# Performance work log

Measured on AMD Instinct MI355X. Metric: run time of the kernel, lower is better.

Reference implementation:

```python
import jax, jax.numpy as jnp
import numpy as np

BATCH = 262144
INPUT_DIM = 256
TREE_DEPTH = 10
NUM_LEAVES = 2 ** TREE_DEPTH


def _leaf_codes(depth):
    # codes[i, d] = d-th most-significant bit of i, matching format(i, f'0{depth}b')
    idx = np.arange(2 ** depth)[:, None]
    shifts = depth - 1 - np.arange(depth)[None, :]
    return jnp.asarray(((idx >> shifts) & 1).astype(np.float32))  # [L, D]


def setup_inputs() -> dict:
    key = jax.random.key(0)
    k1, k2, k3, k4 = jax.random.split(key, 4)
    x = jax.random.normal(k1, (BATCH, INPUT_DIM), dtype=jnp.float32)
    W = jax.random.normal(k2, (INPUT_DIM, TREE_DEPTH), dtype=jnp.float32) * (1.0 / np.sqrt(INPUT_DIM))
    b = jax.random.normal(k3, (TREE_DEPTH,), dtype=jnp.float32) * 0.01
    leaf_values = jax.random.normal(k4, (NUM_LEAVES,), dtype=jnp.float32)
    return {"x": x, "W": W, "b": b, "leaf_values": leaf_values}


def reference(x, W, b, leaf_values):
    depth = W.shape[1]
    codes = _leaf_codes(depth)                      # [L, D]
    decisions = jax.nn.sigmoid(x @ W + b)           # [B, D]
    # prod over depth of (d*c + (1-d)*(1-c)) without a [B, L, D] intermediate:
    # loop over the tiny depth axis (D=10), keeping only [B, L].
    leaf_probs = jnp.ones((x.shape[0], codes.shape[0]), dtype=x.dtype)
    for d in range(depth):
        dd = decisions[:, d][:, None]               # [B, 1]
        cc = codes[:, d][None, :]                   # [1, L]
        leaf_probs = leaf_probs * (dd * cc + (1.0 - dd) * (1.0 - cc))
    out = (leaf_probs * leaf_values).sum(axis=1, keepdims=True)  # [B, 1]
    return out
```

## Files before the change

### kernel.cpp

```cpp
#include <hip/hip_runtime.h>
#include <hip/hip_bf16.h>

#define TD 10
#define NCOL 256
#define GCOLS 32
#define NGRP (NCOL / GCOLS)

template <int LEVEL, int IDX>
__device__ __forceinline__ void fold(const float* __restrict__ lv,
                                     const float (&p)[TD], const float (&q)[TD],
                                     const float (&g)[16],
                                     float prefix, float& acc) {
  if constexpr (LEVEL == TD - 4) {
    const float* l16 = lv + 16 * IDX;
    float t = l16[0] * g[0];
#pragma unroll
    for (int k = 1; k < 16; ++k) t = fmaf(l16[k], g[k], t);
    acc = fmaf(prefix, t, acc);
  } else {
    fold<LEVEL + 1, 2 * IDX>(lv, p, q, g, prefix * q[LEVEL], acc);
    fold<LEVEL + 1, 2 * IDX + 1>(lv, p, q, g, prefix * p[LEVEL], acc);
  }
}

__global__ void __launch_bounds__(256, 4)
odt_kernel(const float* __restrict__ x, const float* __restrict__ W,
           const float* __restrict__ bias, const float* __restrict__ lv,
           float* __restrict__ out) {
  const int row = blockIdx.x * 256 + threadIdx.x;
  const float* __restrict__ xr = x + (size_t)row * NCOL;

  float4 buf[2][8];
#pragma unroll
  for (int j = 0; j < 8; ++j)
    buf[0][j] = *(const float4*)(xr + 4 * j);

  float sums[TD];
#pragma unroll
  for (int d = 0; d < TD; ++d) sums[d] = bias[d];

#pragma unroll
  for (int g = 0; g < NGRP; ++g) {
    if (g + 1 < NGRP) {
#pragma unroll
      for (int j = 0; j < 8; ++j)
        buf[(g + 1) & 1][j] =
            *(const float4*)(xr + (g + 1) * GCOLS + 4 * j);
    }
#pragma unroll
    for (int j = 0; j < 8; ++j) {
#pragma unroll
      for (int e = 0; e < 4; ++e) {
        const float xe = (&buf[g & 1][j].x)[e];
        const int col = g * GCOLS + 4 * j + e;
#pragma unroll
        for (int d = 0; d < TD; ++d)
          sums[d] = fmaf(xe, W[col * TD + d], sums[d]);
      }
    }
  }

  float p[TD], q[TD];
#pragma unroll
  for (int d = 0; d < TD; ++d) {
    const float s = 1.0f / (1.0f + __expf(-sums[d]));
    p[d] = s;
    q[d] = 1.0f - s;
  }

  float g[16];
  {
    float hA[4], hB[4];
    hA[0] = q[6] * q[7]; hA[1] = q[6] * p[7]; hA[2] = p[6] * q[7]; hA[3] = p[6] * p[7];
    hB[0] = q[8] * q[9]; hB[1] = q[8] * p[9]; hB[2] = p[8] * q[9]; hB[3] = p[8] * p[9];
#pragma unroll
    for (int o = 0; o < 16; ++o) g[o] = hA[o >> 2] * hB[o & 3];
  }

  float acc = 0.0f;
  fold<0, 0>(lv, p, q, g, 1.0f, acc);

  out[row] = acc;
}

extern "C" void kernel_launch(void* const* d_in, const int* in_sizes, int n_in,
                              void* d_out, int out_size, void* d_ws, size_t ws_size,
                              hipStream_t stream) {
  const float* x = (const float*)d_in[0];
  const float* W = (const float*)d_in[1];
  const float* b = (const float*)d_in[2];
  const float* lv = (const float*)d_in[3];
  float* out = (float*)d_out;

  const int batch = in_sizes[0] / NCOL;
  const int grid = batch / 256;
  odt_kernel<<<grid, 256, 0, stream>>>(x, W, b, lv, out);
}
```

Measured before the change: 64.64 us.

## Stage x tiles into LDS via direct global-to-LDS loads and split work across waves

Each block now processes 8 tiles of 64 rows. It stages every tile into LDS with global_load_lds, using a rotated column swizzle so that the row-per-lane reads avoid bank conflicts, and prefetches the next tile while the current one is being computed. Each of the 4 waves computes partial dot products over a quarter of the columns, and the partials are reduced through LDS. Each wave also evaluates a quarter of the leaf tree, and those results are summed at the end. The aim is coalesced global reads in place of per-thread strided row loads, plus less redundant per-thread leaf work, at the cost of extra barriers, 64KB+ of LDS and lower occupancy.

```diff
diff --git a/kernel.cpp b/kernel.cpp
--- a/kernel.cpp
+++ b/kernel.cpp
@@ -1,10 +1,16 @@
 #include <hip/hip_runtime.h>
-#include <hip/hip_bf16.h>
 
 #define TD 10
 #define NCOL 256
-#define GCOLS 32
-#define NGRP (NCOL / GCOLS)
+#define TROWS 64
+#define TILES 8
+#define ROWS_PER_BLOCK (TROWS * TILES)
+
+typedef const __attribute__((address_space(1))) void* as1_cvp;
+typedef __attribute__((address_space(3))) void* as3_vp;
+__device__ __forceinline__ void gload_lds16(const float* g, float* l) {
+  __builtin_amdgcn_global_load_lds((as1_cvp)(const void*)g, (as3_vp)(void*)l, 16, 0, 0);
+}
 
 template <int LEVEL, int IDX>
 __device__ __forceinline__ void fold(const float* __restrict__ lv,
@@ -23,64 +29,103 @@
   }
 }
 
-__global__ void __launch_bounds__(256, 4)
+__global__ void __launch_bounds__(256, 2)
 odt_kernel(const float* __restrict__ x, const float* __restrict__ W,
            const float* __restrict__ bias, const float* __restrict__ lv,
            float* __restrict__ out) {
-  const int row = blockIdx.x * 256 + threadIdx.x;
-  const float* __restrict__ xr = x + (size_t)row * NCOL;
+  __shared__ float xt[TROWS * NCOL];
+  __shared__ float ps[4][TROWS][12];
+  __shared__ float accs[4][TROWS];
 
-  float4 buf[2][8];
+  const int lane = threadIdx.x & 63;
+  const int wq = __builtin_amdgcn_readfirstlane(threadIdx.x >> 6);
+  const int blockrow0 = blockIdx.x * ROWS_PER_BLOCK;
+
+  auto stage = [&](int t) {
+    const int trow0 = blockrow0 + t * TROWS;
 #pragma unroll
-  for (int j = 0; j < 8; ++j)
-    buf[0][j] = *(const float4*)(xr + 4 * j);
+    for (int k = 0; k < 16; ++k) {
+      const int r = wq * 16 + k;
+      const float* src = x + (size_t)(trow0 + r) * NCOL + 4 * ((lane - r) & 63);
+      gload_lds16(src, &xt[r * NCOL]);
+    }
+  };
 
-  float sums[TD];
+  stage(0);
+
+  for (int t = 0; t < TILES; ++t) {
+    __syncthreads();
+
+    float sums[TD];
 #pragma unroll
-  for (int d = 0; d < TD; ++d) sums[d] = bias[d];
-
+    for (int d = 0; d < TD; ++d) sums[d] = 0.0f;
 #pragma unroll
-  for (int g = 0; g < NGRP; ++g) {
-    if (g + 1 < NGRP) {
-#pragma unroll
-      for (int j = 0; j < 8; ++j)
-        buf[(g + 1) & 1][j] =
-            *(const float4*)(xr + (g + 1) * GCOLS + 4 * j);
-    }
-#pragma unroll
-    for (int j = 0; j < 8; ++j) {
+    for (int i = 0; i < 16; ++i) {
+      const int pos = (16 * wq + i + lane) & 63;
+      const float4 xv = *(const float4*)&xt[lane * NCOL + 4 * pos];
 #pragma unroll
       for (int e = 0; e < 4; ++e) {
-        const float xe = (&buf[g & 1][j].x)[e];
-        const int col = g * GCOLS + 4 * j + e;
+        const float xe = (&xv.x)[e];
+        const int col = 64 * wq + 4 * i + e;
 #pragma unroll
         for (int d = 0; d < TD; ++d)
           sums[d] = fmaf(xe, W[col * TD + d], sums[d]);
       }
     }
+    {
+      float* pp = &ps[wq][lane][0];
+      *(float4*)(pp)     = make_float4(sums[0], sums[1], sums[2], sums[3]);
+      *(float4*)(pp + 4) = make_float4(sums[4], sums[5], sums[6], sums[7]);
+      *(float2*)(pp + 8) = make_float2(sums[8], sums[9]);
+    }
+
+    __syncthreads();
+
+    if (t + 1 < TILES) stage(t + 1);
+
+    float tot[TD];
+#pragma unroll
+    for (int d = 0; d < TD; ++d) tot[d] = bias[d];
+#pragma unroll
+    for (int wp = 0; wp < 4; ++wp) {
+      const float* qq = &ps[wp][lane][0];
+      const float4 a = *(const float4*)(qq);
+      const float4 b = *(const float4*)(qq + 4);
+      const float2 c = *(const float2*)(qq + 8);
+      tot[0] += a.x; tot[1] += a.y; tot[2] += a.z; tot[3] += a.w;
+      tot[4] += b.x; tot[5] += b.y; tot[6] += b.z; tot[7] += b.w;
+      tot[8] += c.x; tot[9] += c.y;
+    }
+
+    float p[TD], q[TD];
+#pragma unroll
+    for (int d = 0; d < TD; ++d) {
+      const float sg = 1.0f / (1.0f + __expf(-tot[d]));
+      p[d] = sg;
+      q[d] = 1.0f - sg;
+    }
+
+    float g[16];
+    {
+      float hA[4], hB[4];
+      hA[0] = q[6] * q[7]; hA[1] = q[6] * p[7]; hA[2] = p[6] * q[7]; hA[3] = p[6] * p[7];
+      hB[0] = q[8] * q[9]; hB[1] = q[8] * p[9]; hB[2] = p[8] * q[9]; hB[3] = p[8] * p[9];
+#pragma unroll
+      for (int o = 0; o < 16; ++o) g[o] = hA[o >> 2] * hB[o & 3];
+    }
+
+    float acc = 0.0f;
+    const float pref = ((wq & 2) ? p[0] : q[0]) * ((wq & 1) ? p[1] : q[1]);
+    fold<2, 0>(lv + 256 * wq, p, q, g, pref, acc);
+    accs[wq][lane] = acc;
+
+    __syncthreads();
+
+    if (wq == 0) {
+      const float o = accs[0][lane] + accs[1][lane] + accs[2][lane] + accs[3][lane];
+      out[blockrow0 + t * TROWS + lane] = o;
+    }
   }
-
-  float p[TD], q[TD];
-#pragma unroll
-  for (int d = 0; d < TD; ++d) {
-    const float s = 1.0f / (1.0f + __expf(-sums[d]));
-    p[d] = s;
-    q[d] = 1.0f - s;
-  }
-
-  float g[16];
-  {
-    float hA[4], hB[4];
-    hA[0] = q[6] * q[7]; hA[1] = q[6] * p[7]; hA[2] = p[6] * q[7]; hA[3] = p[6] * p[7];
-    hB[0] = q[8] * q[9]; hB[1] = q[8] * p[9]; hB[2] = p[8] * q[9]; hB[3] = p[8] * p[9];
-#pragma unroll
-    for (int o = 0; o < 16; ++o) g[o] = hA[o >> 2] * hB[o & 3];
-  }
-
-  float acc = 0.0f;
-  fold<0, 0>(lv, p, q, g, 1.0f, acc);
-
-  out[row] = acc;
 }
 
 extern "C" void kernel_launch(void* const* d_in, const int* in_sizes, int n_in,
@@ -93,6 +138,6 @@
   float* out = (float*)d_out;
 
   const int batch = in_sizes[0] / NCOL;
-  const int grid = batch / 256;
+  const int grid = batch / ROWS_PER_BLOCK;
   odt_kernel<<<grid, 256, 0, stream>>>(x, W, b, lv, out);
 }
```

Measured after the change: 112.3 us. 73.7% more time.

## Split each row across two waves by column half and leaf subtree

Applied to the files above, without the earlier changes.

Each row is now handled by two threads in different waves. Each thread computes the partial dot product over half of the 256 input columns, and the halves are exchanged through shared memory before the sigmoid. The leaf fold is also split by the first tree level, so each thread evaluates half of the 1024 leaves, and the two partial sums are combined via LDS. This halves the per-thread serial work and register footprint, allowing 8 blocks per CU for more parallelism. In exchange it adds two __syncthreads, LDS traffic, and a duplicated sigmoid computation on both threads of a row.

```diff
diff --git a/kernel.cpp b/kernel.cpp
--- a/kernel.cpp
+++ b/kernel.cpp
@@ -1,10 +1,11 @@
 #include <hip/hip_runtime.h>
-#include <hip/hip_bf16.h>
 
 #define TD 10
 #define NCOL 256
-#define GCOLS 32
-#define NGRP (NCOL / GCOLS)
+#define HALF 128
+#define GCOLS 16
+#define NGRP (HALF / GCOLS)
+#define ROWS_PER_BLOCK 128
 
 template <int LEVEL, int IDX>
 __device__ __forceinline__ void fold(const float* __restrict__ lv,
@@ -23,36 +24,42 @@
   }
 }
 
-__global__ void __launch_bounds__(256, 4)
+__global__ void __launch_bounds__(256, 8)
 odt_kernel(const float* __restrict__ x, const float* __restrict__ W,
            const float* __restrict__ bias, const float* __restrict__ lv,
            float* __restrict__ out) {
-  const int row = blockIdx.x * 256 + threadIdx.x;
-  const float* __restrict__ xr = x + (size_t)row * NCOL;
+  __shared__ float ps[2][ROWS_PER_BLOCK][11];
+  __shared__ float accs[2][ROWS_PER_BLOCK];
 
-  float4 buf[2][8];
+  const int lane = threadIdx.x & 63;
+  const int w = threadIdx.x >> 6;
+  const int h = __builtin_amdgcn_readfirstlane(w >> 1);
+  const int rg = w & 1;
+  const int r = rg * 64 + lane;
+  const int row = blockIdx.x * ROWS_PER_BLOCK + r;
+  const float* __restrict__ xr = x + (size_t)row * NCOL + h * HALF;
+
+  float4 buf[2][4];
 #pragma unroll
-  for (int j = 0; j < 8; ++j)
-    buf[0][j] = *(const float4*)(xr + 4 * j);
+  for (int j = 0; j < 4; ++j) buf[0][j] = *(const float4*)(xr + 4 * j);
 
   float sums[TD];
 #pragma unroll
-  for (int d = 0; d < TD; ++d) sums[d] = bias[d];
+  for (int d = 0; d < TD; ++d) sums[d] = 0.0f;
 
 #pragma unroll
-  for (int g = 0; g < NGRP; ++g) {
-    if (g + 1 < NGRP) {
+  for (int gi = 0; gi < NGRP; ++gi) {
+    if (gi + 1 < NGRP) {
 #pragma unroll
-      for (int j = 0; j < 8; ++j)
-        buf[(g + 1) & 1][j] =
-            *(const float4*)(xr + (g + 1) * GCOLS + 4 * j);
+      for (int j = 0; j < 4; ++j)
+        buf[(gi + 1) & 1][j] = *(const float4*)(xr + (gi + 1) * GCOLS + 4 * j);
     }
 #pragma unroll
-    for (int j = 0; j < 8; ++j) {
+    for (int j = 0; j < 4; ++j) {
 #pragma unroll
       for (int e = 0; e < 4; ++e) {
-        const float xe = (&buf[g & 1][j].x)[e];
-        const int col = g * GCOLS + 4 * j + e;
+        const float xe = (&buf[gi & 1][j].x)[e];
+        const int col = h * HALF + gi * GCOLS + 4 * j + e;
 #pragma unroll
         for (int d = 0; d < TD; ++d)
           sums[d] = fmaf(xe, W[col * TD + d], sums[d]);
@@ -60,12 +67,17 @@
     }
   }
 
+#pragma unroll
+  for (int d = 0; d < TD; ++d) ps[h][r][d] = sums[d];
+  __syncthreads();
+
   float p[TD], q[TD];
 #pragma unroll
   for (int d = 0; d < TD; ++d) {
-    const float s = 1.0f / (1.0f + __expf(-sums[d]));
-    p[d] = s;
-    q[d] = 1.0f - s;
+    const float tot = bias[d] + sums[d] + ps[h ^ 1][r][d];
+    const float sg = 1.0f / (1.0f + __expf(-tot));
+    p[d] = sg;
+    q[d] = 1.0f - sg;
   }
 
   float g[16];
@@ -78,9 +90,13 @@
   }
 
   float acc = 0.0f;
-  fold<0, 0>(lv, p, q, g, 1.0f, acc);
+  if (h == 0) fold<1, 0>(lv, p, q, g, q[0], acc);
+  else        fold<1, 1>(lv, p, q, g, p[0], acc);
+  accs[h][r] = acc;
+  __syncthreads();
 
-  out[row] = acc;
+  if (h == 0)
+    out[row] = accs[0][r] + accs[1][r];
 }
 
 extern "C" void kernel_launch(void* const* d_in, const int* in_sizes, int n_in,
@@ -93,6 +109,6 @@
   float* out = (float*)d_out;
 
   const int batch = in_sizes[0] / NCOL;
-  const int grid = batch / 256;
+  const int grid = batch / ROWS_PER_BLOCK;
   odt_kernel<<<grid, 256, 0, stream>>>(x, W, b, lv, out);
 }
```

Result: slower. 106.8 us (+65.2%).
